# Performance work log

Hardware: AMD Instinct MI355X
Metric: run time of the kernel (lower is better)

## Reference

```python
import jax, jax.numpy as jnp
import numpy as np

B, T, D, H = 4, 2048, 512, 8
DK = D // H


def setup_inputs() -> dict:
    key0 = jax.random.key(0)
    ks = jax.random.split(key0, 16)
    s = 1.0 / np.sqrt(D)
    inp = {
        "query": jax.random.normal(ks[0], (B, T, D), jnp.float32),
        "key": jax.random.normal(ks[1], (B, T, D), jnp.float32),
        "value": jax.random.normal(ks[2], (B, T, D), jnp.float32),
        "mask": jnp.ones((B, 1, T), jnp.int32),
        "pos_emb": jax.random.normal(ks[3], (1, T, D), jnp.float32),
        "Wq": jax.random.normal(ks[4], (D, D), jnp.float32) * s,
        "bq": jnp.zeros((D,), jnp.float32),
        "Wk": jax.random.normal(ks[5], (D, D), jnp.float32) * s,
        "bk": jnp.zeros((D,), jnp.float32),
        "Wv": jax.random.normal(ks[6], (D, D), jnp.float32) * s,
        "bv": jnp.zeros((D,), jnp.float32),
        "Wo": jax.random.normal(ks[7], (D, D), jnp.float32) * s,
        "bo": jnp.zeros((D,), jnp.float32),
        "Wp": jax.random.normal(ks[8], (D, D), jnp.float32) * s,  # linear_pos, no bias
        "pos_bias_u": jax.random.normal(ks[9], (H, DK), jnp.float32) * 0.05,
        "pos_bias_v": jax.random.normal(ks[10], (H, DK), jnp.float32) * 0.05,
    }
    return inp


def reference(query, key, value, mask, pos_emb, Wq, bq, Wk, bk, Wv, bv, Wo, bo, Wp, pos_bias_u, pos_bias_v):
    b, t1, d = query.shape
    h, dk = pos_bias_u.shape
    # projections -> (b, t, h, dk)
    q = (query @ Wq.T + bq).reshape(b, t1, h, dk)
    k = (key @ Wk.T + bk).reshape(b, -1, h, dk)
    v = (value @ Wv.T + bv).reshape(b, -1, h, dk)
    # positional projection (n_batch_pos == 1): (t2, h, dk)
    p = (pos_emb @ Wp.T).reshape(pos_emb.shape[0], -1, h, dk)[0]
    # content score (a+c) and position score (b+d); NOTE: this repo's forward
    # does not apply rel_shift -- matrix_bd is used directly.
    matrix_ac = jnp.einsum("bthd,bshd->bhts", q + pos_bias_u, k)
    matrix_bd = jnp.einsum("bthd,shd->bhts", q + pos_bias_v, p)
    scores = (matrix_ac + matrix_bd) / np.sqrt(dk)
    # mask: (b, 1, t2) -> (b, 1, 1, t2); masked where mask == 0
    m = (mask[:, None, :, :] == 0)
    scores = jnp.where(m, -jnp.inf, scores)
    attn = jax.nn.softmax(scores, axis=-1)
    attn = jnp.where(m, 0.0, attn)
    x = jnp.einsum("bhts,bshd->bthd", attn, v).reshape(b, t1, h * dk)
    return x @ Wo.T + bo
```

## Files before the change

### kernel.cpp

```cpp
#include <hip/hip_runtime.h>

typedef __bf16 bf16;
typedef __attribute__((ext_vector_type(8))) __bf16 bf16x8;
typedef __attribute__((ext_vector_type(4))) __bf16 bf16x4;
typedef __attribute__((ext_vector_type(4))) float f32x4;

#define NB 4
#define NT 2048
#define ND 512
#define NH 8
#define NDK 64
#define GAMMA 0.1803368801111204f

#define OFF_XQ 0ull
#define OFF_XK 4194304ull
#define OFF_XV 8388608ull
#define OFF_XP 12582912ull
#define OFF_WQ 13631488ull
#define OFF_WK 13893632ull
#define OFF_WV 14155776ull
#define OFF_WP 14417920ull
#define OFF_WO 14680064ull
#define OFF_QU 14942208ull
#define OFF_QV 19136512ull
#define OFF_KB 23330816ull
#define OFF_VT 27525120ull
#define OFF_PB 31719424ull
#define OFF_OA OFF_XQ

__global__ __launch_bounds__(256) void convert_bf16(
    const float* __restrict__ q, const float* __restrict__ k,
    const float* __restrict__ v, const float* __restrict__ p,
    const float* __restrict__ wq, const float* __restrict__ wk,
    const float* __restrict__ wv, const float* __restrict__ wp,
    const float* __restrict__ wo, bf16* __restrict__ dst) {
  int bid = blockIdx.x;
  const float* src;
  size_t doff;
  if (bid < 2048) { src = q; doff = OFF_XQ; }
  else if (bid < 4096) { src = k; doff = OFF_XK; bid -= 2048; }
  else if (bid < 6144) { src = v; doff = OFF_XV; bid -= 4096; }
  else if (bid < 6656) { src = p; doff = OFF_XP; bid -= 6144; }
  else if (bid < 6784) { src = wq; doff = OFF_WQ; bid -= 6656; }
  else if (bid < 6912) { src = wk; doff = OFF_WK; bid -= 6784; }
  else if (bid < 7040) { src = wv; doff = OFF_WV; bid -= 6912; }
  else if (bid < 7168) { src = wp; doff = OFF_WP; bid -= 7040; }
  else { src = wo; doff = OFF_WO; bid -= 7168; }
  size_t base = (size_t)bid * 2048 + threadIdx.x * 8;
  float4 x0 = *(const float4*)(src + base);
  float4 x1 = *(const float4*)(src + base + 4);
  bf16x8 o;
  o[0] = (bf16)x0.x; o[1] = (bf16)x0.y; o[2] = (bf16)x0.z; o[3] = (bf16)x0.w;
  o[4] = (bf16)x1.x; o[5] = (bf16)x1.y; o[6] = (bf16)x1.z; o[7] = (bf16)x1.w;
  *(bf16x8*)(dst + doff + base) = o;
}

__device__ __forceinline__ void flush_tile(const bf16* LT, bf16* dst, int bm,
                                           int bn, int tid, bool isP) {
#pragma unroll
  for (int i = 0; i < 8; i++) {
    int chunk = tid + i * 256;
    int mm = chunk >> 4, c8 = (chunk & 15) * 8;
    bf16x8 vv = *(const bf16x8*)&LT[mm * 144 + c8];
    int n = bn + c8, h = n >> 6, d = n & 63;
    int gm = bm + mm;
    size_t gidx;
    if (isP)
      gidx = ((size_t)h * NT + gm) * NDK + d;
    else
      gidx = ((size_t)((gm >> 11) * NH + h) * NT + (gm & 2047)) * NDK + d;
    *(bf16x8*)(dst + gidx) = vv;
  }
}

__global__ __launch_bounds__(256) void proj_fused(
    const bf16* __restrict__ Xq, const bf16* __restrict__ Xk,
    const bf16* __restrict__ Xv, const bf16* __restrict__ Xp,
    const bf16* __restrict__ wq, const bf16* __restrict__ wk,
    const bf16* __restrict__ wv, const bf16* __restrict__ wp,
    const float* __restrict__ bq, const float* __restrict__ bk,
    const float* __restrict__ bv, const float* __restrict__ pu,
    const float* __restrict__ pv, bf16* __restrict__ Qu, bf16* __restrict__ Qv,
    bf16* __restrict__ Kb, bf16* __restrict__ Vt, bf16* __restrict__ Pb) {
  __shared__ bf16 smem[2][128][72];

  const int bid = blockIdx.x;
  const int mode = (bid >= 768) ? 3 : (bid >> 8);
  const int idx = (mode == 3) ? bid - 768 : (bid & 255);
  const int bm = (idx >> 2) * 128, bn = (idx & 3) * 128;

  const bf16* X;
  const bf16* W;
  if (mode == 0) { X = Xq; W = wq; }
  else if (mode == 1) { X = Xk; W = wk; }
  else if (mode == 2) { X = Xv; W = wv; }
  else { X = Xp; W = wp; }

  const int tid = threadIdx.x;
  const int l = tid & 63, w = tid >> 6;
  const int q = l >> 4, ln = l & 15;
  const int wm = (w >> 1) * 64, wn = (w & 1) * 64;

  f32x4 acc[4][4];
#pragma unroll
  for (int i = 0; i < 4; i++)
#pragma unroll
    for (int j = 0; j < 4; j++) acc[i][j] = (f32x4){0.f, 0.f, 0.f, 0.f};

  const int srow = tid >> 3, scol = (tid & 7) * 8;
  const size_t abase = (size_t)(bm + srow) * 512 + scol;
  const size_t bbase = (size_t)(bn + srow) * 512 + scol;

  bf16x8 ar[4], br[4];
#pragma unroll
  for (int i = 0; i < 4; i++) {
    ar[i] = *(const bf16x8*)(X + abase + (size_t)i * 32 * 512);
    br[i] = *(const bf16x8*)(W + bbase + (size_t)i * 32 * 512);
  }

  for (int k0 = 0; k0 < 512; k0 += 64) {
    __syncthreads();
#pragma unroll
    for (int i = 0; i < 4; i++) {
      *(bf16x8*)&smem[0][srow + i * 32][scol] = ar[i];
      *(bf16x8*)&smem[1][srow + i * 32][scol] = br[i];
    }
    if (k0 + 64 < 512) {
#pragma unroll
      for (int i = 0; i < 4; i++) {
        ar[i] = *(const bf16x8*)(X + abase + k0 + 64 + (size_t)i * 32 * 512);
        br[i] = *(const bf16x8*)(W + bbase + k0 + 64 + (size_t)i * 32 * 512);
      }
    }
    __syncthreads();
#pragma unroll
    for (int kc = 0; kc < 2; kc++) {
      bf16x8 af[4], bfr[4];
#pragma unroll
      for (int rt = 0; rt < 4; rt++)
        af[rt] = *(const bf16x8*)&smem[0][wm + rt * 16 + ln][kc * 32 + q * 8];
#pragma unroll
      for (int ct = 0; ct < 4; ct++)
        bfr[ct] = *(const bf16x8*)&smem[1][wn + ct * 16 + ln][kc * 32 + q * 8];
#pragma unroll
      for (int rt = 0; rt < 4; rt++)
#pragma unroll
        for (int ct = 0; ct < 4; ct++)
          acc[rt][ct] = __builtin_amdgcn_mfma_f32_16x16x32_bf16(
              af[rt], bfr[ct], acc[rt][ct], 0, 0, 0);
    }
  }

  bf16* LT = &smem[0][0][0];

  if (mode == 2) {
    __syncthreads();
#pragma unroll
    for (int ct = 0; ct < 4; ct++) {
      const int n = bn + wn + ct * 16 + ln;
      const float bvn = bv[n];
#pragma unroll
      for (int rt = 0; rt < 4; rt++) {
        bf16x4 t4;
#pragma unroll
        for (int r = 0; r < 4; r++) t4[r] = (bf16)(acc[rt][ct][r] + bvn);
        *(bf16x4*)&LT[(wn + ct * 16 + ln) * 144 + wm + rt * 16 + q * 4] = t4;
      }
    }
    __syncthreads();
    const int b = bm >> 11, tb = bm & 2047;
#pragma unroll
    for (int i = 0; i < 8; i++) {
      int chunk = tid + i * 256;
      int nn = chunk >> 4, m8 = (chunk & 15) * 8;
      int n = bn + nn, h = n >> 6, d = n & 63;
      size_t gidx = (((size_t)(b * NH + h)) * NDK + d) * NT + tb + m8;
      *(bf16x8*)(Vt + gidx) = *(const bf16x8*)&LT[nn * 144 + m8];
    }
    return;
  }

  if (mode == 0) {
    float addu[4], addv[4];
#pragma unroll
    for (int ct = 0; ct < 4; ct++) {
      int n = bn + wn + ct * 16 + ln;
      float bb = bq[n];
      addu[ct] = bb + pu[n];
      addv[ct] = bb + pv[n];
    }
    __syncthreads();
#pragma unroll
    for (int rt = 0; rt < 4; rt++)
#pragma unroll
      for (int ct = 0; ct < 4; ct++)
#pragma unroll
        for (int r = 0; r < 4; r++)
          LT[(wm + rt * 16 + q * 4 + r) * 144 + wn + ct * 16 + ln] =
              (bf16)((acc[rt][ct][r] + addu[ct]) * GAMMA);
    __syncthreads();
    flush_tile(LT, Qu, bm, bn, tid, false);
    __syncthreads();
#pragma unroll
    for (int rt = 0; rt < 4; rt++)
#pragma unroll
      for (int ct = 0; ct < 4; ct++)
#pragma unroll
        for (int r = 0; r < 4; r++)
          LT[(wm + rt * 16 + q * 4 + r) * 144 + wn + ct * 16 + ln] =
              (bf16)((acc[rt][ct][r] + addv[ct]) * GAMMA);
    __syncthreads();
    flush_tile(LT, Qv, bm, bn, tid, false);
    return;
  }

  {
    float bb[4];
#pragma unroll
    for (int ct = 0; ct < 4; ct++) {
      int n = bn + wn + ct * 16 + ln;
      bb[ct] = (mode == 1) ? bk[n] : 0.f;
    }
    __syncthreads();
#pragma unroll
    for (int rt = 0; rt < 4; rt++)
#pragma unroll
      for (int ct = 0; ct < 4; ct++)
#pragma unroll
        for (int r = 0; r < 4; r++)
          LT[(wm + rt * 16 + q * 4 + r) * 144 + wn + ct * 16 + ln] =
              (bf16)(acc[rt][ct][r] + bb[ct]);
    __syncthreads();
    flush_tile(LT, (mode == 1) ? Kb : Pb, bm, bn, tid, mode == 3);
  }
}

__global__ __launch_bounds__(256) void flash(
    const bf16* __restrict__ Qu, const bf16* __restrict__ Qv,
    const bf16* __restrict__ Kb, const bf16* __restrict__ Pb,
    const bf16* __restrict__ Vt, const int* __restrict__ mask,
    bf16* __restrict__ Oa) {
  __shared__ bf16 sK[64][136];
  __shared__ bf16 sVt[64][72];
  __shared__ unsigned short sPu[4][16][72];
  __shared__ float sbias[64];

  const int tid = threadIdx.x;
  const int l = tid & 63, w = tid >> 6;
  const int q = l >> 4, ln = l & 15;
  const int t0 = blockIdx.x * 64;
  const int bh = blockIdx.y;
  const int b = bh >> 3;

  const size_t qrow = (((size_t)bh) * NT + t0 + w * 16 + ln) * NDK;
  bf16x8 qf[4];
  qf[0] = *(const bf16x8*)(Qu + qrow + q * 8);
  qf[1] = *(const bf16x8*)(Qu + qrow + 32 + q * 8);
  qf[2] = *(const bf16x8*)(Qv + qrow + q * 8);
  qf[3] = *(const bf16x8*)(Qv + qrow + 32 + q * 8);

  int okacc = 1;
  for (int i = tid; i < NT; i += 256) okacc &= (mask[b * NT + i] != 0);
  const int allones = __syncthreads_and(okacc);

  float lsum[4] = {0.f, 0.f, 0.f, 0.f};
  f32x4 O[4];
#pragma unroll
  for (int dt = 0; dt < 4; dt++) O[dt] = (f32x4){0.f, 0.f, 0.f, 0.f};

  const bf16* Krow = Kb + ((size_t)bh) * NT * NDK;
  const bf16* Prow = Pb + ((size_t)(bh & 7)) * NT * NDK;
  const bf16* Vrow = Vt + ((size_t)bh) * NDK * NT;

  const int krow = tid >> 4, kcc = tid & 15;
  const int vrow = tid >> 3, vcol = (tid & 7) * 8;
  const bf16* kpsrc =
      (kcc < 8) ? (Krow + kcc * 8) : (Prow + (kcc - 8) * 8);

  bf16x8 rk[4], rv[2];
#pragma unroll
  for (int i = 0; i < 4; i++)
    rk[i] = *(const bf16x8*)(kpsrc + (size_t)(krow + i * 16) * NDK);
#pragma unroll
  for (int i = 0; i < 2; i++)
    rv[i] = *(const bf16x8*)(Vrow + (size_t)(vrow + i * 32) * NT + vcol);

  for (int s0 = 0; s0 < NT; s0 += 64) {
    __syncthreads();
#pragma unroll
    for (int i = 0; i < 4; i++) *(bf16x8*)&sK[krow + i * 16][kcc * 8] = rk[i];
#pragma unroll
    for (int i = 0; i < 2; i++) *(bf16x8*)&sVt[vrow + i * 32][vcol] = rv[i];
    if (s0 + 64 < NT) {
#pragma unroll
      for (int i = 0; i < 4; i++)
        rk[i] = *(const bf16x8*)(kpsrc + (size_t)(s0 + 64 + krow + i * 16) * NDK);
#pragma unroll
      for (int i = 0; i < 2; i++)
        rv[i] = *(const bf16x8*)(Vrow + (size_t)(vrow + i * 32) * NT + s0 + 64 +
                                 vcol);
    }
    if (!allones && tid < 64)
      sbias[tid] = mask[b * NT + s0 + tid] ? 0.f : -1e30f;
    __syncthreads();

    f32x4 S[4];
#pragma unroll
    for (int ct = 0; ct < 4; ct++) {
      S[ct] = (f32x4){0.f, 0.f, 0.f, 0.f};
#pragma unroll
      for (int kc = 0; kc < 4; kc++) {
        bf16x8 kf = *(const bf16x8*)&sK[ct * 16 + ln][kc * 32 + q * 8];
        S[ct] = __builtin_amdgcn_mfma_f32_16x16x32_bf16(qf[kc], kf, S[ct], 0,
                                                        0, 0);
      }
    }
    if (!allones) {
#pragma unroll
      for (int ct = 0; ct < 4; ct++) {
        float bc = sbias[ct * 16 + ln];
#pragma unroll
        for (int r = 0; r < 4; r++) S[ct][r] += bc;
      }
    }
#pragma unroll
    for (int ct = 0; ct < 4; ct++) {
#pragma unroll
      for (int r = 0; r < 4; r++) {
        float p = __builtin_amdgcn_exp2f(S[ct][r]);
        unsigned u = __builtin_bit_cast(unsigned, p);
        lsum[r] += __builtin_bit_cast(float, u & 0xffff0000u);
        sPu[w][q * 4 + r][ct * 16 + ln] = (unsigned short)(u >> 16);
      }
    }
    bf16x8 pa0 = *(const bf16x8*)&sPu[w][ln][q * 8];
    bf16x8 pa1 = *(const bf16x8*)&sPu[w][ln][32 + q * 8];
#pragma unroll
    for (int dt = 0; dt < 4; dt++) {
      bf16x8 vb0 = *(const bf16x8*)&sVt[dt * 16 + ln][q * 8];
      bf16x8 vb1 = *(const bf16x8*)&sVt[dt * 16 + ln][32 + q * 8];
      O[dt] = __builtin_amdgcn_mfma_f32_16x16x32_bf16(pa0, vb0, O[dt], 0, 0, 0);
      O[dt] = __builtin_amdgcn_mfma_f32_16x16x32_bf16(pa1, vb1, O[dt], 0, 0, 0);
    }
  }

#pragma unroll
  for (int r = 0; r < 4; r++) {
    float s = lsum[r];
    s += __shfl_xor(s, 1, 16);
    s += __shfl_xor(s, 2, 16);
    s += __shfl_xor(s, 4, 16);
    s += __shfl_xor(s, 8, 16);
    float inv = (s > 0.f) ? 1.f / s : 0.f;
    int t = t0 + w * 16 + q * 4 + r;
    size_t base = (((size_t)b * NT + t) * NH + (bh & 7)) * NDK;
#pragma unroll
    for (int dt = 0; dt < 4; dt++)
      Oa[base + dt * 16 + ln] = (bf16)(O[dt][r] * inv);
  }
}

__global__ __launch_bounds__(256) void out_gemm(const bf16* __restrict__ A,
                                                const bf16* __restrict__ W,
                                                const float* __restrict__ bias,
                                                float* __restrict__ out) {
  __shared__ bf16 sA[128][72];
  __shared__ bf16 sB[64][72];

  const int tid = threadIdx.x;
  const int l = tid & 63, w = tid >> 6;
  const int q = l >> 4, ln = l & 15;
  const int wm = (w >> 1) * 64, wn = (w & 1) * 32;
  const int bm = blockIdx.x * 128, bn = blockIdx.y * 64;

  f32x4 acc[4][2];
#pragma unroll
  for (int i = 0; i < 4; i++)
#pragma unroll
    for (int j = 0; j < 2; j++) acc[i][j] = (f32x4){0.f, 0.f, 0.f, 0.f};

  const int srow = tid >> 3, scol = (tid & 7) * 8;
  const size_t abase = (size_t)(bm + srow) * 512 + scol;
  const size_t bbase = (size_t)(bn + srow) * 512 + scol;

  bf16x8 ar[4], br[2];
#pragma unroll
  for (int i = 0; i < 4; i++)
    ar[i] = *(const bf16x8*)(A + abase + (size_t)i * 32 * 512);
#pragma unroll
  for (int i = 0; i < 2; i++)
    br[i] = *(const bf16x8*)(W + bbase + (size_t)i * 32 * 512);

  for (int k0 = 0; k0 < 512; k0 += 64) {
    __syncthreads();
#pragma unroll
    for (int i = 0; i < 4; i++) *(bf16x8*)&sA[srow + i * 32][scol] = ar[i];
#pragma unroll
    for (int i = 0; i < 2; i++) *(bf16x8*)&sB[srow + i * 32][scol] = br[i];
    if (k0 + 64 < 512) {
#pragma unroll
      for (int i = 0; i < 4; i++)
        ar[i] = *(const bf16x8*)(A + abase + k0 + 64 + (size_t)i * 32 * 512);
#pragma unroll
      for (int i = 0; i < 2; i++)
        br[i] = *(const bf16x8*)(W + bbase + k0 + 64 + (size_t)i * 32 * 512);
    }
    __syncthreads();
#pragma unroll
    for (int kc = 0; kc < 2; kc++) {
      bf16x8 af[4], bfr[2];
#pragma unroll
      for (int rt = 0; rt < 4; rt++)
        af[rt] = *(const bf16x8*)&sA[wm + rt * 16 + ln][kc * 32 + q * 8];
#pragma unroll
      for (int ct = 0; ct < 2; ct++)
        bfr[ct] = *(const bf16x8*)&sB[wn + ct * 16 + ln][kc * 32 + q * 8];
#pragma unroll
      for (int rt = 0; rt < 4; rt++)
#pragma unroll
        for (int ct = 0; ct < 2; ct++)
          acc[rt][ct] = __builtin_amdgcn_mfma_f32_16x16x32_bf16(
              af[rt], bfr[ct], acc[rt][ct], 0, 0, 0);
    }
  }

#pragma unroll
  for (int rt = 0; rt < 4; rt++)
#pragma unroll
    for (int ct = 0; ct < 2; ct++) {
      const int n = bn + wn + ct * 16 + ln;
      const float bias_n = bias[n];
#pragma unroll
      for (int r = 0; r < 4; r++) {
        const int m = bm + wm + rt * 16 + q * 4 + r;
        out[(size_t)m * 512 + n] = acc[rt][ct][r] + bias_n;
      }
    }
}

extern "C" void kernel_launch(void* const* d_in, const int* in_sizes, int n_in,
                              void* d_out, int out_size, void* d_ws,
                              size_t ws_size, hipStream_t stream) {
  const float* query = (const float*)d_in[0];
  const float* key = (const float*)d_in[1];
  const float* value = (const float*)d_in[2];
  const int* mask = (const int*)d_in[3];
  const float* pos = (const float*)d_in[4];
  const float* Wq = (const float*)d_in[5];
  const float* bq = (const float*)d_in[6];
  const float* Wk = (const float*)d_in[7];
  const float* bk = (const float*)d_in[8];
  const float* Wv = (const float*)d_in[9];
  const float* bv = (const float*)d_in[10];
  const float* Wo = (const float*)d_in[11];
  const float* bo = (const float*)d_in[12];
  const float* Wp = (const float*)d_in[13];
  const float* pu = (const float*)d_in[14];
  const float* pv = (const float*)d_in[15];
  float* out = (float*)d_out;

  bf16* ws = (bf16*)d_ws;
  dim3 blk(256);
  convert_bf16<<<dim3(7296), blk, 0, stream>>>(query, key, value, pos, Wq, Wk,
                                               Wv, Wp, Wo, ws);
  proj_fused<<<dim3(832), blk, 0, stream>>>(
      ws + OFF_XQ, ws + OFF_XK, ws + OFF_XV, ws + OFF_XP, ws + OFF_WQ,
      ws + OFF_WK, ws + OFF_WV, ws + OFF_WP, bq, bk, bv, pu, pv, ws + OFF_QU,
      ws + OFF_QV, ws + OFF_KB, ws + OFF_VT, ws + OFF_PB);
  flash<<<dim3(32, 32), blk, 0, stream>>>(ws + OFF_QU, ws + OFF_QV,
                                          ws + OFF_KB, ws + OFF_PB,
                                          ws + OFF_VT, mask, ws + OFF_OA);
  out_gemm<<<dim3(64, 8), blk, 0, stream>>>(ws + OFF_OA, ws + OFF_WO, bo, out);
}
```

Before: 260.8 us.

## Compute transposed score tiles so P is written packed to LDS

Swaps the MFMA operands so each lane holds four consecutive key columns of a single query row. Probabilities can then be packed into 64-bit LDS stores, and the row sum becomes one scalar accumulated per lane, finished with two cross-lane shuffles. The P staging buffer shrinks to a 32-column half, processed in two chunks. This is meant to cut LDS store count and bank traffic in the softmax-to-PV handoff, at the cost of reusing the smaller buffer within each iteration.

New measurement: 248.0 us. -4.9%, faster.

```diff
diff --git a/kernel.cpp b/kernel.cpp
--- a/kernel.cpp
+++ b/kernel.cpp
@@ -242,7 +242,7 @@
     bf16* __restrict__ Oa) {
   __shared__ bf16 sK[64][136];
   __shared__ bf16 sVt[64][72];
-  __shared__ unsigned short sPu[4][16][72];
+  __shared__ bf16 sPT[4][16][40];
   __shared__ float sbias[64];
 
   const int tid = threadIdx.x;
@@ -263,7 +263,7 @@
   for (int i = tid; i < NT; i += 256) okacc &= (mask[b * NT + i] != 0);
   const int allones = __syncthreads_and(okacc);
 
-  float lsum[4] = {0.f, 0.f, 0.f, 0.f};
+  float lsum = 0.f;
   f32x4 O[4];
 #pragma unroll
   for (int dt = 0; dt < 4; dt++) O[dt] = (f32x4){0.f, 0.f, 0.f, 0.f};
@@ -274,8 +274,7 @@
 
   const int krow = tid >> 4, kcc = tid & 15;
   const int vrow = tid >> 3, vcol = (tid & 7) * 8;
-  const bf16* kpsrc =
-      (kcc < 8) ? (Krow + kcc * 8) : (Prow + (kcc - 8) * 8);
+  const bf16* kpsrc = (kcc < 8) ? (Krow + kcc * 8) : (Prow + (kcc - 8) * 8);
 
   bf16x8 rk[4], rv[2];
 #pragma unroll
@@ -294,7 +293,8 @@
     if (s0 + 64 < NT) {
 #pragma unroll
       for (int i = 0; i < 4; i++)
-        rk[i] = *(const bf16x8*)(kpsrc + (size_t)(s0 + 64 + krow + i * 16) * NDK);
+        rk[i] =
+            *(const bf16x8*)(kpsrc + (size_t)(s0 + 64 + krow + i * 16) * NDK);
 #pragma unroll
       for (int i = 0; i < 2; i++)
         rv[i] = *(const bf16x8*)(Vrow + (size_t)(vrow + i * 32) * NT + s0 + 64 +
@@ -304,54 +304,66 @@
       sbias[tid] = mask[b * NT + s0 + tid] ? 0.f : -1e30f;
     __syncthreads();
 
-    f32x4 S[4];
+    f32x4 ST[4];
 #pragma unroll
     for (int ct = 0; ct < 4; ct++) {
-      S[ct] = (f32x4){0.f, 0.f, 0.f, 0.f};
+      ST[ct] = (f32x4){0.f, 0.f, 0.f, 0.f};
 #pragma unroll
       for (int kc = 0; kc < 4; kc++) {
         bf16x8 kf = *(const bf16x8*)&sK[ct * 16 + ln][kc * 32 + q * 8];
-        S[ct] = __builtin_amdgcn_mfma_f32_16x16x32_bf16(qf[kc], kf, S[ct], 0,
-                                                        0, 0);
+        ST[ct] = __builtin_amdgcn_mfma_f32_16x16x32_bf16(kf, qf[kc], ST[ct], 0,
+                                                         0, 0);
       }
     }
     if (!allones) {
 #pragma unroll
       for (int ct = 0; ct < 4; ct++) {
-        float bc = sbias[ct * 16 + ln];
-#pragma unroll
-        for (int r = 0; r < 4; r++) S[ct][r] += bc;
-      }
-    }
-#pragma unroll
-    for (int ct = 0; ct < 4; ct++) {
-#pragma unroll
-      for (int r = 0; r < 4; r++) {
-        float p = __builtin_amdgcn_exp2f(S[ct][r]);
-        unsigned u = __builtin_bit_cast(unsigned, p);
-        lsum[r] += __builtin_bit_cast(float, u & 0xffff0000u);
-        sPu[w][q * 4 + r][ct * 16 + ln] = (unsigned short)(u >> 16);
-      }
-    }
-    bf16x8 pa0 = *(const bf16x8*)&sPu[w][ln][q * 8];
-    bf16x8 pa1 = *(const bf16x8*)&sPu[w][ln][32 + q * 8];
-#pragma unroll
-    for (int dt = 0; dt < 4; dt++) {
-      bf16x8 vb0 = *(const bf16x8*)&sVt[dt * 16 + ln][q * 8];
-      bf16x8 vb1 = *(const bf16x8*)&sVt[dt * 16 + ln][32 + q * 8];
-      O[dt] = __builtin_amdgcn_mfma_f32_16x16x32_bf16(pa0, vb0, O[dt], 0, 0, 0);
-      O[dt] = __builtin_amdgcn_mfma_f32_16x16x32_bf16(pa1, vb1, O[dt], 0, 0, 0);
-    }
-  }
-
+        float4 bb = *(const float4*)&sbias[ct * 16 + q * 4];
+        ST[ct][0] += bb.x;
+        ST[ct][1] += bb.y;
+        ST[ct][2] += bb.z;
+        ST[ct][3] += bb.w;
+      }
+    }
+#pragma unroll
+    for (int c = 0; c < 2; c++) {
+#pragma unroll
+      for (int cc = 0; cc < 2; cc++) {
+        const int ct = c * 2 + cc;
+        unsigned u0 = __builtin_bit_cast(unsigned,
+                                         __builtin_amdgcn_exp2f(ST[ct][0]));
+        unsigned u1 = __builtin_bit_cast(unsigned,
+                                         __builtin_amdgcn_exp2f(ST[ct][1]));
+        unsigned u2 = __builtin_bit_cast(unsigned,
+                                         __builtin_amdgcn_exp2f(ST[ct][2]));
+        unsigned u3 = __builtin_bit_cast(unsigned,
+                                         __builtin_amdgcn_exp2f(ST[ct][3]));
+        lsum += __builtin_bit_cast(float, u0 & 0xffff0000u) +
+                __builtin_bit_cast(float, u1 & 0xffff0000u) +
+                __builtin_bit_cast(float, u2 & 0xffff0000u) +
+                __builtin_bit_cast(float, u3 & 0xffff0000u);
+        uint2 pk;
+        pk.x = (u0 >> 16) | (u1 & 0xffff0000u);
+        pk.y = (u2 >> 16) | (u3 & 0xffff0000u);
+        *(uint2*)&sPT[w][ln][cc * 16 + q * 4] = pk;
+      }
+      bf16x8 paf = *(const bf16x8*)&sPT[w][ln][q * 8];
+#pragma unroll
+      for (int dt = 0; dt < 4; dt++) {
+        bf16x8 vb = *(const bf16x8*)&sVt[dt * 16 + ln][c * 32 + q * 8];
+        O[dt] =
+            __builtin_amdgcn_mfma_f32_16x16x32_bf16(paf, vb, O[dt], 0, 0, 0);
+      }
+    }
+  }
+
+  float s = lsum;
+  s += __shfl_xor(s, 16);
+  s += __shfl_xor(s, 32);
 #pragma unroll
   for (int r = 0; r < 4; r++) {
-    float s = lsum[r];
-    s += __shfl_xor(s, 1, 16);
-    s += __shfl_xor(s, 2, 16);
-    s += __shfl_xor(s, 4, 16);
-    s += __shfl_xor(s, 8, 16);
-    float inv = (s > 0.f) ? 1.f / s : 0.f;
+    float dr = __shfl(s, q * 4 + r);
+    float inv = (dr > 0.f) ? 1.f / dr : 0.f;
     int t = t0 + w * 16 + q * 4 + r;
     size_t base = (((size_t)b * NT + t) * NH + (bh & 7)) * NDK;
 #pragma unroll
```
